# Performance work log

Hardware: AMD Instinct MI355X
Metric: run time of the kernel (lower is better)

Reference implementation:

```python
import jax, jax.numpy as jnp
import numpy as np

B, L, D, H = 2, 2048, 1024, 16
DK = D // H


def setup_inputs() -> dict:
    key = jax.random.key(0)
    ks = jax.random.split(key, 11)
    s = 0.02
    return {
        "q": jax.random.normal(ks[0], (B, L, D), jnp.float32),
        "k": jax.random.normal(ks[1], (B, L, D), jnp.float32),
        "v": jax.random.normal(ks[2], (B, L, D), jnp.float32),
        "mask": jnp.ones((B, 1, 1, L), jnp.int32),
        "wq": jax.random.normal(ks[3], (D, D), jnp.float32) * s,
        "bq": jnp.zeros((D,), jnp.float32),
        "wk": jax.random.normal(ks[4], (D, D), jnp.float32) * s,
        "bk": jnp.zeros((D,), jnp.float32),
        "wv": jax.random.normal(ks[5], (D, D), jnp.float32) * s,
        "bv": jnp.zeros((D,), jnp.float32),
        "wo": jax.random.normal(ks[6], (D, D), jnp.float32) * s,
        "bo": jnp.zeros((D,), jnp.float32),
    }


def _split_heads(x):
    # (B, L, D) -> (B, H, L, DK)
    return x.reshape(B, L, H, DK).transpose(0, 2, 1, 3)


def reference(q, k, v, mask, wq, bq, wk, bk, wv, bv, wo, bo):
    query = _split_heads(q @ wq.T + bq)
    key = _split_heads(k @ wk.T + bk)
    value = _split_heads(v @ wv.T + bv)
    scale = 1.0 / jnp.sqrt(jnp.asarray(DK, query.dtype))
    # (B, H, Lq, Lk) materialized scores, as in the original module
    scores = jnp.einsum('bhqd,bhkd->bhqk', query, key) * scale
    scores = jnp.where(mask == 0, jnp.asarray(-1e9, scores.dtype), scores)
    weights = jax.nn.softmax(scores, axis=-1)
    out = jnp.einsum('bhqk,bhkd->bhqd', weights, value)
    out = out.transpose(0, 2, 1, 3).reshape(B, L, D)
    return out @ wo.T + bo
```

## Files before the change

kernel.cpp:

```cpp
#include <hip/hip_runtime.h>
#include <hip/hip_bf16.h>


#define DEVINL __device__ __forceinline__

typedef __attribute__((ext_vector_type(8))) short short8;
typedef __attribute__((ext_vector_type(4))) float floatx4;

static constexpr int Bq = 2, Lq = 2048, Dm = 1024;
static constexpr int Mrows = Bq * Lq;
static constexpr size_t QKV_LD = 3072;
static constexpr int NT = Lq / 64;

DEVINL unsigned short f2bf(float x) {
  __hip_bfloat16 h = __float2bfloat16(x);
  unsigned short u;
  __builtin_memcpy(&u, &h, 2);
  return u;
}

DEVINL float bf2f(unsigned short u) {
  unsigned int t = ((unsigned int)u) << 16;
  float f;
  __builtin_memcpy(&f, &t, 4);
  return f;
}

DEVINL short8 cvt8(float4 a, float4 b) {
  union { unsigned short u[8]; short8 v; } o;
  o.u[0] = f2bf(a.x); o.u[1] = f2bf(a.y); o.u[2] = f2bf(a.z); o.u[3] = f2bf(a.w);
  o.u[4] = f2bf(b.x); o.u[5] = f2bf(b.y); o.u[6] = f2bf(b.z); o.u[7] = f2bf(b.w);
  return o.v;
}

DEVINL void gll16(const void* g, const void* l) {
  auto gp = (const __attribute__((address_space(1))) char*)(unsigned long long)(uintptr_t)g;
  auto lp = (__attribute__((address_space(3))) char*)(unsigned int)(uintptr_t)l;
  __builtin_amdgcn_global_load_lds(gp, lp, 16, 0, 0);
}

template <bool A_BF16, bool OUT_BF16>
__global__ __launch_bounds__(256) void gemm_k(
    const void* __restrict__ A0, const void* __restrict__ A1, const void* __restrict__ A2,
    const float* __restrict__ W0, const float* __restrict__ W1, const float* __restrict__ W2,
    const float* __restrict__ b0, const float* __restrict__ b1, const float* __restrict__ b2,
    void* __restrict__ Cout, int M, int N, int K, int ldc) {
  const int bid = blockIdx.x;
  const int xcd = bid & 7, sl = bid >> 3;
  const int g = xcd + ((sl >> 3) << 3), jn = sl & 7;
  const int z = g >> 5;
  const int m0 = (g & 31) * 128, n0 = jn * 128;

  const void* Aany = (z == 0) ? A0 : ((z == 1) ? A1 : A2);
  const float* W = (z == 0) ? W0 : ((z == 1) ? W1 : W2);
  const float* bias = (z == 0) ? b0 : ((z == 1) ? b1 : b2);
  const int tid = threadIdx.x, lane = tid & 63, w = tid >> 6;
  const int wr = w >> 1, wc = w & 1;

  __shared__ __align__(16) unsigned short As[2][128 * 32];
  __shared__ __align__(16) unsigned short Bs[2][128 * 32];

  floatx4 acc[4][4] = {};
  float4 wreg[2][2], areg[2][2];

  auto loadW = [&](int kt) {
#pragma unroll
    for (int it = 0; it < 2; ++it) {
      int gg = it * 256 + tid, row = gg >> 2, gk = gg & 3;
      const float* p = W + (size_t)(n0 + row) * K + kt + gk * 8;
      wreg[it][0] = ((const float4*)p)[0];
      wreg[it][1] = ((const float4*)p)[1];
    }
  };
  auto loadA = [&](int kt) {
#pragma unroll
    for (int it = 0; it < 2; ++it) {
      int gg = it * 256 + tid, row = gg >> 2, gk = gg & 3;
      const float* p = (const float*)Aany + (size_t)(m0 + row) * K + kt + gk * 8;
      areg[it][0] = ((const float4*)p)[0];
      areg[it][1] = ((const float4*)p)[1];
    }
  };
  auto writeW = [&](int buf) {
#pragma unroll
    for (int it = 0; it < 2; ++it) {
      int gg = it * 256 + tid, row = gg >> 2, gk = gg & 3;
      *(short8*)((char*)Bs + buf * 8192 + row * 64 + ((gk ^ (row & 3)) << 4)) =
          cvt8(wreg[it][0], wreg[it][1]);
    }
  };
  auto writeA = [&](int buf) {
#pragma unroll
    for (int it = 0; it < 2; ++it) {
      int gg = it * 256 + tid, row = gg >> 2, gk = gg & 3;
      *(short8*)((char*)As + buf * 8192 + row * 64 + ((gk ^ (row & 3)) << 4)) =
          cvt8(areg[it][0], areg[it][1]);
    }
  };
  auto stageA = [&](int kt, int buf) {
#pragma unroll
    for (int it = 0; it < 2; ++it) {
      int gg = it * 256 + tid, row = gg >> 2, gk = gg & 3;
      int koff = (gk ^ (row & 3)) * 8;
      gll16((const unsigned short*)Aany + (size_t)(m0 + row) * K + kt + koff,
            (const char*)As + buf * 8192 + (it * 256 + w * 64) * 16);
    }
  };

  const int nt = K / 32;
  loadW(0);
  if (!A_BF16) loadA(0);
  writeW(0);
  if (A_BF16) stageA(0, 0); else writeA(0);
  if (nt > 1) { loadW(32); if (!A_BF16) loadA(32); }
  __syncthreads();

  const int krow = lane >> 4;
  for (int t = 0; t < nt; ++t) {
    const int c = t & 1, n = c ^ 1;
    short8 af[4], bfr[4];
#pragma unroll
    for (int m = 0; m < 4; ++m) {
      int row = wr * 64 + m * 16 + (lane & 15);
      af[m] = *(const short8*)((const char*)As + c * 8192 + row * 64 + ((krow ^ (row & 3)) << 4));
    }
#pragma unroll
    for (int n2 = 0; n2 < 4; ++n2) {
      int row = wc * 64 + n2 * 16 + (lane & 15);
      bfr[n2] = *(const short8*)((const char*)Bs + c * 8192 + row * 64 + ((krow ^ (row & 3)) << 4));
    }
    if (t + 1 < nt) {
      writeW(n);
      if (A_BF16) stageA((t + 1) * 32, n); else writeA(n);
      if (t + 2 < nt) { loadW((t + 2) * 32); if (!A_BF16) loadA((t + 2) * 32); }
    }
    __builtin_amdgcn_s_setprio(1);
#pragma unroll
    for (int m = 0; m < 4; ++m)
#pragma unroll
      for (int n2 = 0; n2 < 4; ++n2)
        acc[m][n2] = __builtin_amdgcn_mfma_f32_16x16x32_bf16(af[m], bfr[n2], acc[m][n2], 0, 0, 0);
    __builtin_amdgcn_s_setprio(0);
    __syncthreads();
  }

  const int r4 = lane >> 4;
#pragma unroll
  for (int m = 0; m < 4; ++m)
#pragma unroll
    for (int n2 = 0; n2 < 4; ++n2) {
      int col = n0 + wc * 64 + n2 * 16 + (lane & 15);
      float bv = bias[col];
#pragma unroll
      for (int r = 0; r < 4; ++r) {
        int row = m0 + wr * 64 + m * 16 + r4 * 4 + r;
        float v = acc[m][n2][r] + bv;
        if (OUT_BF16)
          ((unsigned short*)Cout)[(size_t)row * ldc + (size_t)z * N + col] = f2bf(v);
        else
          ((float*)Cout)[(size_t)row * ldc + (size_t)z * N + col] = v;
      }
    }
}

__global__ __launch_bounds__(256) void attn_kernel(const unsigned short* __restrict__ QKV,
                                                   const int* __restrict__ mask,
                                                   unsigned short* __restrict__ Aout) {
  const int bid = blockIdx.x;
  const int xcd = bid & 7, sl = bid >> 3;
  const int bh = xcd + ((sl >> 5) << 3);
  const int q0 = (sl & 31) * 64;
  const int b = bh >> 4, h = bh & 15;
  const int tid = threadIdx.x, lane = tid & 63, w = tid >> 6;

  __shared__ __align__(16) unsigned short Klds[2][64 * 64];
  __shared__ __align__(16) unsigned short Vtlds[2][64 * 64];
  __shared__ __align__(16) unsigned short Plds[4][16 * 64];
  __shared__ int mflag[NT];

  const unsigned short* base = QKV + (size_t)b * Lq * QKV_LD;
  const unsigned short* Kbase = base + 1024;
  const unsigned short* Vbase = base + 2048;

  const int kp = tid & 31;
  const int vd0 = (tid >> 5) * 8;

  auto stageK = [&](int t, int buf) {
#pragma unroll
    for (int it = 0; it < 2; ++it) {
      int g = it * 256 + tid, key = g >> 3, gk = g & 7;
      gll16(Kbase + (size_t)(t * 64 + key) * QKV_LD + h * 64 + (gk ^ (key & 7)) * 8,
            (const char*)Klds + buf * 8192 + (it * 256 + w * 64) * 16);
    }
  };
  short8 vr0, vr1;
  auto loadV = [&](int t) {
    vr0 = *(const short8*)(Vbase + (size_t)(t * 64 + 2 * kp) * QKV_LD + h * 64 + vd0);
    vr1 = *(const short8*)(Vbase + (size_t)(t * 64 + 2 * kp + 1) * QKV_LD + h * 64 + vd0);
  };
  auto writeV = [&](int buf) {
#pragma unroll
    for (int i = 0; i < 8; ++i) {
      int d = vd0 + i;
      unsigned int val = (unsigned int)(unsigned short)vr0[i] |
                         ((unsigned int)(unsigned short)vr1[i] << 16);
      *(unsigned int*)((char*)Vtlds + buf * 8192 + d * 128 + (((kp >> 2) ^ (d & 7)) << 4) +
                       (kp & 3) * 4) = val;
    }
  };

  stageK(0, 0);
  loadV(0);
  writeV(0);
  {
    const int* mp = mask + b * Lq + tid * 8;
    int4 a = ((const int4*)mp)[0], bb = ((const int4*)mp)[1];
    int myall = (a.x && a.y && a.z && a.w && bb.x && bb.y && bb.z && bb.w) ? 1 : 0;
    unsigned long long bal = __ballot(myall);
    if (lane < 8) mflag[w * 8 + lane] = (((bal >> (lane * 8)) & 0xffull) == 0xffull);
  }

  short8 qf[2];
  {
    int row = q0 + w * 16 + (lane & 15);
#pragma unroll
    for (int c = 0; c < 2; ++c) {
      short8 raw = *(const short8*)(base + (size_t)row * QKV_LD + h * 64 + c * 32 + (lane >> 4) * 8);
      union { unsigned short u[8]; short8 v; } o2;
#pragma unroll
      for (int i = 0; i < 8; ++i) o2.u[i] = f2bf(bf2f((unsigned short)raw[i]) * 0.18033688f);
      qf[c] = o2.v;
    }
  }
  union { unsigned short u[8]; short8 v; } one_u;
#pragma unroll
  for (int i = 0; i < 8; ++i) one_u.u[i] = 0x3F80;
  const short8 ones8 = one_u.v;

  __syncthreads();

  floatx4 o[4] = {};
  floatx4 lacc = {};
  float mrow[4];
#pragma unroll
  for (int r = 0; r < 4; ++r) mrow[r] = -1e30f;

  for (int t = 0; t < NT; ++t) {
    const int c = t & 1, n = c ^ 1;
    if (t + 1 < NT) { stageK(t + 1, n); loadV(t + 1); }

    floatx4 s[4] = {};
    __builtin_amdgcn_s_setprio(1);
#pragma unroll
    for (int f = 0; f < 4; ++f) {
      int key = f * 16 + (lane & 15);
#pragma unroll
      for (int c2 = 0; c2 < 2; ++c2) {
        short8 kf = *(const short8*)((const char*)Klds + c * 8192 + key * 128 +
                                     (((c2 * 4 + (lane >> 4)) ^ (key & 7)) << 4));
        s[f] = __builtin_amdgcn_mfma_f32_16x16x32_bf16(qf[c2], kf, s[f], 0, 0, 0);
      }
    }
    __builtin_amdgcn_s_setprio(0);

    float tmax[4];
#pragma unroll
    for (int r = 0; r < 4; ++r)
      tmax[r] = fmaxf(fmaxf(s[0][r], s[1][r]), fmaxf(s[2][r], s[3][r]));
    const int allm = mflag[t];
    bool ok = (tmax[0] <= mrow[0] + 11.5f) && (tmax[1] <= mrow[1] + 11.5f) &&
              (tmax[2] <= mrow[2] + 11.5f) && (tmax[3] <= mrow[3] + 11.5f);
    if (__ballot(ok && allm) == ~0ull) {
#pragma unroll
      for (int f = 0; f < 4; ++f)
#pragma unroll
        for (int r = 0; r < 4; ++r) s[f][r] = __builtin_amdgcn_exp2f(s[f][r] - mrow[r]);
    } else {
#pragma unroll
      for (int dx = 1; dx <= 8; dx <<= 1)
#pragma unroll
        for (int r = 0; r < 4; ++r) tmax[r] = fmaxf(tmax[r], __shfl_xor(tmax[r], dx, 64));
      float mnew[4], alpha[4];
#pragma unroll
      for (int r = 0; r < 4; ++r) {
        mnew[r] = fmaxf(mrow[r], tmax[r]);
        alpha[r] = __builtin_amdgcn_exp2f(mrow[r] - mnew[r]);
        mrow[r] = mnew[r];
      }
#pragma unroll
      for (int df = 0; df < 4; ++df)
#pragma unroll
        for (int r = 0; r < 4; ++r) o[df][r] *= alpha[r];
#pragma unroll
      for (int r = 0; r < 4; ++r) lacc[r] *= alpha[r];
      if (allm) {
#pragma unroll
        for (int f = 0; f < 4; ++f)
#pragma unroll
          for (int r = 0; r < 4; ++r) s[f][r] = __builtin_amdgcn_exp2f(s[f][r] - mnew[r]);
      } else {
#pragma unroll
        for (int f = 0; f < 4; ++f) {
          int mv = mask[b * Lq + t * 64 + f * 16 + (lane & 15)];
#pragma unroll
          for (int r = 0; r < 4; ++r)
            s[f][r] = mv ? __builtin_amdgcn_exp2f(s[f][r] - mnew[r]) : 0.f;
        }
      }
    }

#pragma unroll
    for (int f = 0; f < 4; ++f)
#pragma unroll
      for (int r = 0; r < 4; ++r) {
        int row = (lane >> 4) * 4 + r, col = f * 16 + (lane & 15);
        *(unsigned short*)((char*)&Plds[w][0] + row * 128 + (((col >> 3) ^ (row & 7)) << 4) +
                           (col & 7) * 2) = f2bf(s[f][r]);
      }

    short8 pf[2];
#pragma unroll
    for (int kc = 0; kc < 2; ++kc)
      pf[kc] = *(const short8*)((const char*)&Plds[w][0] + (lane & 15) * 128 +
                                (((kc * 4 + (lane >> 4)) ^ (lane & 7)) << 4));
    __builtin_amdgcn_s_setprio(1);
    lacc = __builtin_amdgcn_mfma_f32_16x16x32_bf16(pf[0], ones8, lacc, 0, 0, 0);
    lacc = __builtin_amdgcn_mfma_f32_16x16x32_bf16(pf[1], ones8, lacc, 0, 0, 0);
#pragma unroll
    for (int df = 0; df < 4; ++df) {
      int d = df * 16 + (lane & 15);
#pragma unroll
      for (int kc = 0; kc < 2; ++kc) {
        short8 vf = *(const short8*)((const char*)Vtlds + c * 8192 + d * 128 +
                                     (((kc * 4 + (lane >> 4)) ^ (d & 7)) << 4));
        o[df] = __builtin_amdgcn_mfma_f32_16x16x32_bf16(pf[kc], vf, o[df], 0, 0, 0);
      }
    }
    __builtin_amdgcn_s_setprio(0);

    if (t + 1 < NT) writeV(n);
    __syncthreads();
  }

  float rl[4];
#pragma unroll
  for (int r = 0; r < 4; ++r) rl[r] = 1.0f / lacc[r];
#pragma unroll
  for (int df = 0; df < 4; ++df)
#pragma unroll
    for (int r = 0; r < 4; ++r) {
      int row = q0 + w * 16 + (lane >> 4) * 4 + r;
      int col = h * 64 + df * 16 + (lane & 15);
      Aout[(size_t)(b * Lq + row) * Dm + col] = f2bf(o[df][r] * rl[r]);
    }
}

extern "C" void kernel_launch(void* const* d_in, const int* in_sizes, int n_in,
                              void* d_out, int out_size, void* d_ws, size_t ws_size,
                              hipStream_t stream) {
  const float* q = (const float*)d_in[0];
  const float* k = (const float*)d_in[1];
  const float* v = (const float*)d_in[2];
  const int* maskp = (const int*)d_in[3];
  const float* wq = (const float*)d_in[4];
  const float* bq = (const float*)d_in[5];
  const float* wk = (const float*)d_in[6];
  const float* bk = (const float*)d_in[7];
  const float* wv = (const float*)d_in[8];
  const float* bv = (const float*)d_in[9];
  const float* wo = (const float*)d_in[10];
  const float* bo = (const float*)d_in[11];

  unsigned short* qkv = (unsigned short*)d_ws;
  unsigned short* attnout = qkv + (size_t)Mrows * QKV_LD;

  gemm_k<false, true><<<dim3(768), 256, 0, stream>>>(
      q, k, v, wq, wk, wv, bq, bk, bv, qkv, Mrows, Dm, Dm, (int)QKV_LD);

  attn_kernel<<<dim3(1024), 256, 0, stream>>>(qkv, maskp, attnout);

  gemm_k<true, false><<<dim3(256), 256, 0, stream>>>(
      attnout, attnout, attnout, wo, wo, wo, bo, bo, bo, d_out, Mrows, Dm, Dm, Dm);
}
```

Baseline: 278.3 us.

## Pre-cast QKV inputs to bf16 and stage A via direct global-to-LDS loads

Adds a separate cast kernel that converts q, k and v from fp32 to bf16 into scratch space, using the output buffer and workspace. The QKV projection GEMM can then load A through global_load_lds instead of loading fp32 into registers and converting. The A staging and next W write are also moved to the top of the loop, ahead of the fragment reads. The cost is an extra kernel launch and a full fp32 read plus bf16 write pass over the inputs. In exchange the GEMM reads half the A bytes and needs fewer registers.

```diff
diff --git a/kernel.cpp b/kernel.cpp
--- a/kernel.cpp
+++ b/kernel.cpp
@@ -39,9 +39,25 @@
   __builtin_amdgcn_global_load_lds(gp, lp, 16, 0, 0);
 }
 
-template <bool A_BF16, bool OUT_BF16>
+__global__ __launch_bounds__(256) void cast3(const float* __restrict__ q,
+                                             const float* __restrict__ k,
+                                             const float* __restrict__ v,
+                                             unsigned short* __restrict__ dq,
+                                             unsigned short* __restrict__ dk,
+                                             unsigned short* __restrict__ dv) {
+  const int z = blockIdx.y;
+  const float* s = (z == 0) ? q : ((z == 1) ? k : v);
+  unsigned short* d = (z == 0) ? dq : ((z == 1) ? dk : dv);
+  int i = blockIdx.x * 256 + threadIdx.x;
+  float4 a = ((const float4*)s)[i * 2];
+  float4 b = ((const float4*)s)[i * 2 + 1];
+  ((short8*)d)[i] = cvt8(a, b);
+}
+
+template <bool OUT_BF16>
 __global__ __launch_bounds__(256) void gemm_k(
-    const void* __restrict__ A0, const void* __restrict__ A1, const void* __restrict__ A2,
+    const unsigned short* __restrict__ A0, const unsigned short* __restrict__ A1,
+    const unsigned short* __restrict__ A2,
     const float* __restrict__ W0, const float* __restrict__ W1, const float* __restrict__ W2,
     const float* __restrict__ b0, const float* __restrict__ b1, const float* __restrict__ b2,
     void* __restrict__ Cout, int M, int N, int K, int ldc) {
@@ -51,7 +67,7 @@
   const int z = g >> 5;
   const int m0 = (g & 31) * 128, n0 = jn * 128;
 
-  const void* Aany = (z == 0) ? A0 : ((z == 1) ? A1 : A2);
+  const unsigned short* A = (z == 0) ? A0 : ((z == 1) ? A1 : A2);
   const float* W = (z == 0) ? W0 : ((z == 1) ? W1 : W2);
   const float* bias = (z == 0) ? b0 : ((z == 1) ? b1 : b2);
   const int tid = threadIdx.x, lane = tid & 63, w = tid >> 6;
@@ -61,7 +77,7 @@
   __shared__ __align__(16) unsigned short Bs[2][128 * 32];
 
   floatx4 acc[4][4] = {};
-  float4 wreg[2][2], areg[2][2];
+  float4 wreg[2][2];
 
   auto loadW = [&](int kt) {
 #pragma unroll
@@ -72,15 +88,6 @@
       wreg[it][1] = ((const float4*)p)[1];
     }
   };
-  auto loadA = [&](int kt) {
-#pragma unroll
-    for (int it = 0; it < 2; ++it) {
-      int gg = it * 256 + tid, row = gg >> 2, gk = gg & 3;
-      const float* p = (const float*)Aany + (size_t)(m0 + row) * K + kt + gk * 8;
-      areg[it][0] = ((const float4*)p)[0];
-      areg[it][1] = ((const float4*)p)[1];
-    }
-  };
   auto writeW = [&](int buf) {
 #pragma unroll
     for (int it = 0; it < 2; ++it) {
@@ -89,35 +96,31 @@
           cvt8(wreg[it][0], wreg[it][1]);
     }
   };
-  auto writeA = [&](int buf) {
-#pragma unroll
-    for (int it = 0; it < 2; ++it) {
-      int gg = it * 256 + tid, row = gg >> 2, gk = gg & 3;
-      *(short8*)((char*)As + buf * 8192 + row * 64 + ((gk ^ (row & 3)) << 4)) =
-          cvt8(areg[it][0], areg[it][1]);
-    }
-  };
   auto stageA = [&](int kt, int buf) {
 #pragma unroll
     for (int it = 0; it < 2; ++it) {
       int gg = it * 256 + tid, row = gg >> 2, gk = gg & 3;
       int koff = (gk ^ (row & 3)) * 8;
-      gll16((const unsigned short*)Aany + (size_t)(m0 + row) * K + kt + koff,
+      gll16(A + (size_t)(m0 + row) * K + kt + koff,
             (const char*)As + buf * 8192 + (it * 256 + w * 64) * 16);
     }
   };
 
   const int nt = K / 32;
   loadW(0);
-  if (!A_BF16) loadA(0);
+  stageA(0, 0);
   writeW(0);
-  if (A_BF16) stageA(0, 0); else writeA(0);
-  if (nt > 1) { loadW(32); if (!A_BF16) loadA(32); }
+  if (nt > 1) loadW(32);
   __syncthreads();
 
   const int krow = lane >> 4;
   for (int t = 0; t < nt; ++t) {
     const int c = t & 1, n = c ^ 1;
+    if (t + 1 < nt) {
+      stageA((t + 1) * 32, n);
+      writeW(n);
+      if (t + 2 < nt) loadW((t + 2) * 32);
+    }
     short8 af[4], bfr[4];
 #pragma unroll
     for (int m = 0; m < 4; ++m) {
@@ -128,11 +131,6 @@
     for (int n2 = 0; n2 < 4; ++n2) {
       int row = wc * 64 + n2 * 16 + (lane & 15);
       bfr[n2] = *(const short8*)((const char*)Bs + c * 8192 + row * 64 + ((krow ^ (row & 3)) << 4));
-    }
-    if (t + 1 < nt) {
-      writeW(n);
-      if (A_BF16) stageA((t + 1) * 32, n); else writeA(n);
-      if (t + 2 < nt) { loadW((t + 2) * 32); if (!A_BF16) loadA((t + 2) * 32); }
     }
     __builtin_amdgcn_s_setprio(1);
 #pragma unroll
@@ -371,14 +369,21 @@
   const float* wo = (const float*)d_in[10];
   const float* bo = (const float*)d_in[11];
 
-  unsigned short* qkv = (unsigned short*)d_ws;
-  unsigned short* attnout = qkv + (size_t)Mrows * QKV_LD;
-
-  gemm_k<false, true><<<dim3(768), 256, 0, stream>>>(
-      q, k, v, wq, wk, wv, bq, bk, bv, qkv, Mrows, Dm, Dm, (int)QKV_LD);
+  const size_t nIn = (size_t)Mrows * Dm;
+
+  unsigned short* q_bf = (unsigned short*)d_out;
+  unsigned short* k_bf = q_bf + nIn;
+  unsigned short* v_bf = (unsigned short*)d_ws;
+  unsigned short* qkv = v_bf + nIn;
+  unsigned short* attnout = (unsigned short*)d_ws;
+
+  cast3<<<dim3(nIn / 8 / 256, 3), 256, 0, stream>>>(q, k, v, q_bf, k_bf, v_bf);
+
+  gemm_k<true><<<dim3(768), 256, 0, stream>>>(
+      q_bf, k_bf, v_bf, wq, wk, wv, bq, bk, bv, qkv, Mrows, Dm, Dm, (int)QKV_LD);
 
   attn_kernel<<<dim3(1024), 256, 0, stream>>>(qkv, maskp, attnout);
 
-  gemm_k<true, false><<<dim3(256), 256, 0, stream>>>(
+  gemm_k<false><<<dim3(256), 256, 0, stream>>>(
       attnout, attnout, attnout, wo, wo, wo, bo, bo, bo, d_out, Mrows, Dm, Dm, Dm);
 }
```

Measured after the change: 279.1 us. About the same (+0.3%).
